# Optimization experiments

Measured on AMD Instinct MI355X. Metric: run time of the kernel, lower is better.

Reference implementation:

```python
import jax, jax.numpy as jnp
import numpy as np

V, E, U, L = 50000, 512, 20, 9   # vocab, embed dim, user feats, labels
R, S, T = 64, 32, 50             # reviews, sentences/review, tokens/sentence
D = E + U                        # product-encoder input dim


def setup_inputs() -> dict:
    key = jax.random.key(0)
    ks = jax.random.split(key, 16)
    sc = lambda k, shape: (jax.random.normal(k, shape, jnp.float32) * 0.02)
    return {
        "inputs": jax.random.randint(ks[0], (R, S, T), 0, V),
        "user_feats": jax.random.normal(ks[1], (R, U), jnp.float32),
        "embedding": sc(ks[2], (V, E)),
        "w_sent": sc(ks[3], (E, E)), "b_sent": jnp.zeros((E,), jnp.float32),
        "w_rev": sc(ks[4], (E, E)),  "b_rev": jnp.zeros((E,), jnp.float32),
        "w_prod": sc(ks[5], (D, D)), "b_prod": jnp.zeros((D,), jnp.float32),
        "w_rff": sc(ks[6], (D, 1)),  "b_rff": jnp.zeros((1,), jnp.float32),
        "w_pff": sc(ks[7], (D, L)),  "b_pff": jnp.zeros((L,), jnp.float32),
        "user_w": jnp.ones((U,), jnp.float32),
    }


def _masked_mean(x, mask):
    # x: [..., N, F], mask: [..., N] -> [..., F]
    denom = jnp.maximum(mask.sum(-1, keepdims=True), 1.0)
    return (x * mask[..., None]).sum(-2) / denom


def reference(inputs, user_feats, embedding, w_sent, b_sent, w_rev, b_rev,
              w_prod, b_prod, w_rff, b_rff, w_pff, b_pff, user_w):
    dt = embedding.dtype
    tok_mask = (inputs != 0).astype(dt)                      # [R,S,T]
    emb = embedding[inputs]                                  # [R,S,T,E]
    # sentence encoder (DAN): masked mean over tokens + Linear + SELU
    sent_h = jax.nn.selu(_masked_mean(emb, tok_mask) @ w_sent + b_sent)   # [R,S,E]
    # review encoder: masked mean over sentences (r_mask = p.sum(-1) != 0)
    sent_mask = (inputs.sum(-1) != 0).astype(dt)             # [R,S]
    rev_h = jax.nn.selu(_masked_mean(sent_h, sent_mask) @ w_rev + b_rev)  # [R,E]
    # append L2-normalized user feats scaled by learned weights
    norm = jnp.sqrt((user_feats * user_feats).sum(-1, keepdims=True))
    uf = user_feats / jnp.maximum(norm, 1e-12) * user_w      # [R,U]
    p_batch = jnp.concatenate([rev_h, uf], axis=-1)          # [R,D]
    # per-review star head
    r_stars = jax.nn.selu(p_batch @ w_rff + b_rff).squeeze(-1)            # [R]
    # product encoder: plain mean over reviews (no mask) + Linear + SELU
    h_n = jax.nn.selu(p_batch.mean(-2) @ w_prod + b_prod)    # [D]
    p_stars = jax.nn.selu(h_n @ w_pff + b_pff)               # [L]
    return p_stars, r_stars
```

## Files before the change

kernel.cpp:

```cpp
#include <hip/hip_runtime.h>
#include <hip/hip_bf16.h>

#define R_ 64
#define S_ 32
#define T_ 50
#define E_ 512
#define U_ 20
#define D_ 532
#define L_ 9
#define NSENT (R_ * S_)

#define PCHUNK 128
#define NCG 5
#define NKG 5

typedef __attribute__((ext_vector_type(8))) short bf16x8;
typedef __attribute__((ext_vector_type(4))) float f32x4;

__device__ __forceinline__ float selu_f(float x) {
    const float scale = 1.0507009873554805f;
    const float alpha = 1.6732632423543772f;
    return x > 0.0f ? scale * x : scale * alpha * expm1f(x);
}

__device__ __forceinline__ void store_out(float* p, float v) { *p = v; }
__device__ __forceinline__ void store_out(__hip_bfloat16* p, float v) { *p = __float2bfloat16(v); }

__global__ __launch_bounds__(256) void k_sent_mean(
        const int* __restrict__ inputs,
        const float* __restrict__ emb,
        __hip_bfloat16* __restrict__ sent_bf,
        float* __restrict__ smask)
{
    const int sid = blockIdx.x;
    const int tid = threadIdx.x;
    const int base = sid * T_;
    float2 acc = {0.f, 0.f};
    int cnt = 0;
    int idsum = 0;
    for (int t = 0; t < T_; ++t) {
        int tok = inputs[base + t];
        idsum += tok;
        if (tok != 0) {
            ++cnt;
            float2 v = ((const float2*)(emb + (size_t)tok * E_))[tid];
            acc.x += v.x; acc.y += v.y;
        }
    }
    const float denom = fmaxf((float)cnt, 1.0f);
    __hip_bfloat162 h2;
    h2.x = __float2bfloat16(acc.x / denom);
    h2.y = __float2bfloat16(acc.y / denom);
    ((__hip_bfloat162*)(sent_bf + (size_t)sid * E_))[tid] = h2;
    if (tid == 0) smask[sid] = (idsum != 0) ? 1.0f : 0.0f;
}

__global__ __launch_bounds__(256) void k_cvt_wT(
        const float* __restrict__ w_sent,
        const float* __restrict__ w_rev,
        __hip_bfloat16* __restrict__ wT)
{
    const float* w = blockIdx.z ? w_rev : w_sent;
    __hip_bfloat16* o = wT + (size_t)blockIdx.z * E_ * E_;
    __shared__ float tile[32][33];
    const int tx = threadIdx.x & 31, ty = threadIdx.x >> 5;
    const int k0 = blockIdx.y * 32, n0 = blockIdx.x * 32;
    #pragma unroll
    for (int i = 0; i < 4; ++i)
        tile[ty + 8 * i][tx] = w[(size_t)(k0 + ty + 8 * i) * E_ + n0 + tx];
    __syncthreads();
    #pragma unroll
    for (int i = 0; i < 4; ++i)
        o[(size_t)(n0 + ty + 8 * i) * E_ + k0 + tx] = __float2bfloat16(tile[tx][ty + 8 * i]);
}

template <typename OutT>
__global__ __launch_bounds__(256) void k_gemm_selu(
        const __hip_bfloat16* __restrict__ A,
        const __hip_bfloat16* __restrict__ Bt,
        const float* __restrict__ bias,
        OutT* __restrict__ C, int ldc)
{
    __shared__ short As[64][40];
    __shared__ short Bs[64][40];
    const int tid  = threadIdx.x;
    const int wid  = tid >> 6;
    const int lane = tid & 63;
    const int wm = wid >> 1, wn = wid & 1;
    const int bm = blockIdx.y * 64, bn = blockIdx.x * 64;

    const int srow = tid >> 2;
    const int soff = (tid & 3) * 8;

    const short* Ag  = (const short*)A;
    const short* Btg = (const short*)Bt;

    f32x4 acc[2][2];
    #pragma unroll
    for (int i = 0; i < 2; ++i)
        #pragma unroll
        for (int j = 0; j < 2; ++j) acc[i][j] = (f32x4){0.f, 0.f, 0.f, 0.f};

    const int fr = lane & 15;
    const int kg = (lane >> 4) * 8;

    for (int k0 = 0; k0 < E_; k0 += 32) {
        __syncthreads();
        *(bf16x8*)&As[srow][soff] = *(const bf16x8*)&Ag[(size_t)(bm + srow) * E_ + k0 + soff];
        *(bf16x8*)&Bs[srow][soff] = *(const bf16x8*)&Btg[(size_t)(bn + srow) * E_ + k0 + soff];
        __syncthreads();
        bf16x8 af0 = *(const bf16x8*)&As[wm * 32 + fr][kg];
        bf16x8 af1 = *(const bf16x8*)&As[wm * 32 + 16 + fr][kg];
        bf16x8 bf0 = *(const bf16x8*)&Bs[wn * 32 + fr][kg];
        bf16x8 bf1 = *(const bf16x8*)&Bs[wn * 32 + 16 + fr][kg];
        acc[0][0] = __builtin_amdgcn_mfma_f32_16x16x32_bf16(af0, bf0, acc[0][0], 0, 0, 0);
        acc[0][1] = __builtin_amdgcn_mfma_f32_16x16x32_bf16(af0, bf1, acc[0][1], 0, 0, 0);
        acc[1][0] = __builtin_amdgcn_mfma_f32_16x16x32_bf16(af1, bf0, acc[1][0], 0, 0, 0);
        acc[1][1] = __builtin_amdgcn_mfma_f32_16x16x32_bf16(af1, bf1, acc[1][1], 0, 0, 0);
    }

    const int rq = (lane >> 4) * 4;
    #pragma unroll
    for (int fm = 0; fm < 2; ++fm) {
        #pragma unroll
        for (int fn = 0; fn < 2; ++fn) {
            const int col = bn + wn * 32 + fn * 16 + fr;
            const float bv = bias[col];
            #pragma unroll
            for (int j = 0; j < 4; ++j) {
                const int row = bm + wm * 32 + fm * 16 + rq + j;
                store_out(&C[(size_t)row * ldc + col], selu_f(acc[fm][fn][j] + bv));
            }
        }
    }
}

__global__ __launch_bounds__(256) void k_rev_mean(
        const __hip_bfloat16* __restrict__ sent_h,
        const float* __restrict__ smask,
        __hip_bfloat16* __restrict__ mrev)
{
    const int r = blockIdx.x;
    const int tid = threadIdx.x;
    float2 acc = {0.f, 0.f};
    float msum = 0.f;
    for (int s = 0; s < S_; ++s) {
        const float m = smask[r * S_ + s];
        __hip_bfloat162 v = ((const __hip_bfloat162*)(sent_h + (size_t)(r * S_ + s) * E_))[tid];
        acc.x = fmaf(__bfloat162float(v.x), m, acc.x);
        acc.y = fmaf(__bfloat162float(v.y), m, acc.y);
        msum += m;
    }
    const float denom = fmaxf(msum, 1.0f);
    __hip_bfloat162 h2;
    h2.x = __float2bfloat16(acc.x / denom);
    h2.y = __float2bfloat16(acc.y / denom);
    ((__hip_bfloat162*)(mrev + (size_t)r * E_))[tid] = h2;
}

__global__ __launch_bounds__(64) void k_pbatch(
        const float* __restrict__ user_feats,
        const float* __restrict__ user_w,
        const float* __restrict__ w_rff,
        const float* __restrict__ b_rff,
        float* __restrict__ p_batch,
        float* __restrict__ out_r)
{
    __shared__ float uf[U_];
    const int r = blockIdx.x;
    const int tid = threadIdx.x;
    if (tid < U_) {
        float ss = 0.f;
        #pragma unroll
        for (int j = 0; j < U_; ++j) {
            const float u = user_feats[r * U_ + j];
            ss = fmaf(u, u, ss);
        }
        const float nrm = fmaxf(sqrtf(ss), 1e-12f);
        const float v = user_feats[r * U_ + tid] / nrm * user_w[tid];
        uf[tid] = v;
        p_batch[(size_t)r * D_ + E_ + tid] = v;
    }
    __syncthreads();
    float part = 0.f;
    #pragma unroll
    for (int i = 0; i < 8; ++i)
        part = fmaf(p_batch[(size_t)r * D_ + tid + 64 * i], w_rff[tid + 64 * i], part);
    if (tid < U_) part = fmaf(uf[tid], w_rff[E_ + tid], part);
    #pragma unroll
    for (int off = 32; off > 0; off >>= 1) part += __shfl_down(part, off, 64);
    if (tid == 0) out_r[r] = selu_f(part + b_rff[0]);
}

__global__ __launch_bounds__(256) void k_prod_partial(
        const float* __restrict__ p_batch,
        const float* __restrict__ w_prod,
        float* __restrict__ part)
{
    __shared__ float pbar[PCHUNK];
    __shared__ float red[2][PCHUNK];
    const int cg = blockIdx.x, kg = blockIdx.y;
    const int tid = threadIdx.x;
    const int cl = tid & (PCHUNK - 1);
    const int h  = tid >> 7;
    const int k0 = kg * PCHUNK;
    const int klen = min(PCHUNK, D_ - k0);

    if (cl < klen) {
        float s = 0.f;
        #pragma unroll 8
        for (int r = h * 32; r < h * 32 + 32; ++r)
            s += p_batch[(size_t)r * D_ + k0 + cl];
        red[h][cl] = s;
    }
    __syncthreads();
    if (h == 0 && cl < klen) pbar[cl] = (red[0][cl] + red[1][cl]) * (1.0f / 64.0f);
    __syncthreads();

    const int c = cg * PCHUNK + cl;
    float acc = 0.f;
    if (c < D_) {
        const int jb = h * 64;
        const int je = min(jb + 64, klen);
        for (int j = jb; j < je; ++j)
            acc = fmaf(pbar[j], w_prod[(size_t)(k0 + j) * D_ + c], acc);
    }
    red[h][cl] = acc;
    __syncthreads();
    if (h == 0 && c < D_) part[kg * D_ + c] = red[0][cl] + red[1][cl];
}

__global__ __launch_bounds__(256) void k_prod_final(
        const float* __restrict__ part,
        const float* __restrict__ b_prod,
        const float* __restrict__ w_pff,
        const float* __restrict__ b_pff,
        float* __restrict__ out_p)
{
    __shared__ float hn[D_];
    const int tid = threadIdx.x;
    for (int c = tid; c < D_; c += 256) {
        float s = b_prod[c];
        #pragma unroll
        for (int kg = 0; kg < NKG; ++kg) s += part[kg * D_ + c];
        hn[c] = selu_f(s);
    }
    __syncthreads();
    if (tid < L_) {
        float a = 0.f;
        for (int k = 0; k < D_; ++k) a = fmaf(hn[k], w_pff[k * L_ + tid], a);
        out_p[tid] = selu_f(a + b_pff[tid]);
    }
}

extern "C" void kernel_launch(void* const* d_in, const int* in_sizes, int n_in,
                              void* d_out, int out_size, void* d_ws, size_t ws_size,
                              hipStream_t stream) {
    const int*   inputs     = (const int*)  d_in[0];
    const float* user_feats = (const float*)d_in[1];
    const float* emb        = (const float*)d_in[2];
    const float* w_sent     = (const float*)d_in[3];
    const float* b_sent     = (const float*)d_in[4];
    const float* w_rev      = (const float*)d_in[5];
    const float* b_rev      = (const float*)d_in[6];
    const float* w_prod     = (const float*)d_in[7];
    const float* b_prod     = (const float*)d_in[8];
    const float* w_rff      = (const float*)d_in[9];
    const float* b_rff      = (const float*)d_in[10];
    const float* w_pff      = (const float*)d_in[11];
    const float* b_pff      = (const float*)d_in[12];
    const float* user_w     = (const float*)d_in[13];
    float* out = (float*)d_out;

    float* ws = (float*)d_ws;
    __hip_bfloat16* sent_bf  = (__hip_bfloat16*)(ws);
    __hip_bfloat16* sent_hbf = (__hip_bfloat16*)(ws + 524288);
    __hip_bfloat16* wT       = (__hip_bfloat16*)(ws + 1048576);
    __hip_bfloat16* mrev     = (__hip_bfloat16*)(ws + 1310720);
    float* smask   = ws + 1327104;
    float* p_batch = ws + 1329152;
    float* part    = ws + 1363200;

    k_sent_mean<<<NSENT, 256, 0, stream>>>(inputs, emb, sent_bf, smask);
    k_cvt_wT<<<dim3(16, 16, 2), 256, 0, stream>>>(w_sent, w_rev, wT);
    k_gemm_selu<__hip_bfloat16><<<dim3(E_ / 64, NSENT / 64), 256, 0, stream>>>(
        sent_bf, wT, b_sent, sent_hbf, E_);
    k_rev_mean<<<R_, 256, 0, stream>>>(sent_hbf, smask, mrev);
    k_gemm_selu<float><<<dim3(E_ / 64, R_ / 64), 256, 0, stream>>>(
        mrev, wT + (size_t)E_ * E_, b_rev, p_batch, D_);
    k_pbatch<<<R_, 64, 0, stream>>>(user_feats, user_w, w_rff, b_rff, p_batch, out + L_);
    k_prod_partial<<<dim3(NCG, NKG), 256, 0, stream>>>(p_batch, w_prod, part);
    k_prod_final<<<1, 256, 0, stream>>>(part, b_prod, w_pff, b_pff, out);
}
```

Before: 81.89 us.

## Fuse sentence mean with weight transpose and fold review GEMM into review kernel

```diff
diff --git a/kernel.cpp b/kernel.cpp
--- a/kernel.cpp
+++ b/kernel.cpp
@@ -23,63 +23,72 @@
     return x > 0.0f ? scale * x : scale * alpha * expm1f(x);
 }
 
-__device__ __forceinline__ void store_out(float* p, float v) { *p = v; }
-__device__ __forceinline__ void store_out(__hip_bfloat16* p, float v) { *p = __float2bfloat16(v); }
-
-__global__ __launch_bounds__(256) void k_sent_mean(
+__global__ __launch_bounds__(256) void k_fused_A(
         const int* __restrict__ inputs,
         const float* __restrict__ emb,
+        const float* __restrict__ w_sent,
         __hip_bfloat16* __restrict__ sent_bf,
+        __hip_bfloat16* __restrict__ wT,
         float* __restrict__ smask)
 {
+    __shared__ float red[2][E_];
+    __shared__ int scnt[2], ssum[2];
+    __shared__ float tile[32][33];
+    const int tid = threadIdx.x;
+
+    if (blockIdx.x >= NSENT) {
+        const int b = blockIdx.x - NSENT;
+        const int tx = tid & 31, ty = tid >> 5;
+        const int k0 = (b >> 4) * 32, n0 = (b & 15) * 32;
+        #pragma unroll
+        for (int i = 0; i < 4; ++i)
+            tile[ty + 8 * i][tx] = w_sent[(size_t)(k0 + ty + 8 * i) * E_ + n0 + tx];
+        __syncthreads();
+        #pragma unroll
+        for (int i = 0; i < 4; ++i)
+            wT[(size_t)(n0 + ty + 8 * i) * E_ + k0 + tx] = __float2bfloat16(tile[tx][ty + 8 * i]);
+        return;
+    }
+
     const int sid = blockIdx.x;
-    const int tid = threadIdx.x;
-    const int base = sid * T_;
-    float2 acc = {0.f, 0.f};
-    int cnt = 0;
-    int idsum = 0;
-    for (int t = 0; t < T_; ++t) {
-        int tok = inputs[base + t];
+    const int c4 = (tid & 127) * 4;
+    const int half = tid >> 7;
+    float4 acc = {0.f, 0.f, 0.f, 0.f};
+    int cnt = 0, idsum = 0;
+    #pragma unroll
+    for (int t = half; t < T_; t += 2) {
+        const int tok = inputs[sid * T_ + t];
+        const float m = (tok != 0) ? 1.0f : 0.0f;
+        cnt += (tok != 0);
         idsum += tok;
-        if (tok != 0) {
-            ++cnt;
-            float2 v = ((const float2*)(emb + (size_t)tok * E_))[tid];
-            acc.x += v.x; acc.y += v.y;
-        }
-    }
-    const float denom = fmaxf((float)cnt, 1.0f);
-    __hip_bfloat162 h2;
-    h2.x = __float2bfloat16(acc.x / denom);
-    h2.y = __float2bfloat16(acc.y / denom);
-    ((__hip_bfloat162*)(sent_bf + (size_t)sid * E_))[tid] = h2;
-    if (tid == 0) smask[sid] = (idsum != 0) ? 1.0f : 0.0f;
-}
-
-__global__ __launch_bounds__(256) void k_cvt_wT(
-        const float* __restrict__ w_sent,
-        const float* __restrict__ w_rev,
-        __hip_bfloat16* __restrict__ wT)
-{
-    const float* w = blockIdx.z ? w_rev : w_sent;
-    __hip_bfloat16* o = wT + (size_t)blockIdx.z * E_ * E_;
-    __shared__ float tile[32][33];
-    const int tx = threadIdx.x & 31, ty = threadIdx.x >> 5;
-    const int k0 = blockIdx.y * 32, n0 = blockIdx.x * 32;
-    #pragma unroll
-    for (int i = 0; i < 4; ++i)
-        tile[ty + 8 * i][tx] = w[(size_t)(k0 + ty + 8 * i) * E_ + n0 + tx];
-    __syncthreads();
-    #pragma unroll
-    for (int i = 0; i < 4; ++i)
-        o[(size_t)(n0 + ty + 8 * i) * E_ + k0 + tx] = __float2bfloat16(tile[tx][ty + 8 * i]);
-}
-
-template <typename OutT>
+        const float4 v = *(const float4*)(emb + (size_t)tok * E_ + c4);
+        acc.x = fmaf(v.x, m, acc.x);
+        acc.y = fmaf(v.y, m, acc.y);
+        acc.z = fmaf(v.z, m, acc.z);
+        acc.w = fmaf(v.w, m, acc.w);
+    }
+    *(float4*)&red[half][c4] = acc;
+    if ((tid & 127) == 0) { scnt[half] = cnt; ssum[half] = idsum; }
+    __syncthreads();
+    if (half == 0) {
+        const float4 a = *(const float4*)&red[0][c4];
+        const float4 b = *(const float4*)&red[1][c4];
+        const float inv = 1.0f / fmaxf((float)(scnt[0] + scnt[1]), 1.0f);
+        union { ushort4 u; __hip_bfloat16 h[4]; } o;
+        o.h[0] = __float2bfloat16((a.x + b.x) * inv);
+        o.h[1] = __float2bfloat16((a.y + b.y) * inv);
+        o.h[2] = __float2bfloat16((a.z + b.z) * inv);
+        o.h[3] = __float2bfloat16((a.w + b.w) * inv);
+        *((ushort4*)(sent_bf + (size_t)sid * E_) + (tid & 127)) = o.u;
+        if (tid == 0) smask[sid] = ((ssum[0] + ssum[1]) != 0) ? 1.0f : 0.0f;
+    }
+}
+
 __global__ __launch_bounds__(256) void k_gemm_selu(
         const __hip_bfloat16* __restrict__ A,
         const __hip_bfloat16* __restrict__ Bt,
         const float* __restrict__ bias,
-        OutT* __restrict__ C, int ldc)
+        __hip_bfloat16* __restrict__ C, int ldc)
 {
     __shared__ short As[64][40];
     __shared__ short Bs[64][40];
@@ -129,36 +138,17 @@
             #pragma unroll
             for (int j = 0; j < 4; ++j) {
                 const int row = bm + wm * 32 + fm * 16 + rq + j;
-                store_out(&C[(size_t)row * ldc + col], selu_f(acc[fm][fn][j] + bv));
+                C[(size_t)row * ldc + col] = __float2bfloat16(selu_f(acc[fm][fn][j] + bv));
             }
         }
     }
 }
 
-__global__ __launch_bounds__(256) void k_rev_mean(
+__global__ __launch_bounds__(256) void k_rev_fused(
         const __hip_bfloat16* __restrict__ sent_h,
         const float* __restrict__ smask,
-        __hip_bfloat16* __restrict__ mrev)
-{
-    const int r = blockIdx.x;
-    const int tid = threadIdx.x;
-    float2 acc = {0.f, 0.f};
-    float msum = 0.f;
-    for (int s = 0; s < S_; ++s) {
-        const float m = smask[r * S_ + s];
-        __hip_bfloat162 v = ((const __hip_bfloat162*)(sent_h + (size_t)(r * S_ + s) * E_))[tid];
-        acc.x = fmaf(__bfloat162float(v.x), m, acc.x);
-        acc.y = fmaf(__bfloat162float(v.y), m, acc.y);
-        msum += m;
-    }
-    const float denom = fmaxf(msum, 1.0f);
-    __hip_bfloat162 h2;
-    h2.x = __float2bfloat16(acc.x / denom);
-    h2.y = __float2bfloat16(acc.y / denom);
-    ((__hip_bfloat162*)(mrev + (size_t)r * E_))[tid] = h2;
-}
-
-__global__ __launch_bounds__(64) void k_pbatch(
+        const float* __restrict__ w_rev,
+        const float* __restrict__ b_rev,
         const float* __restrict__ user_feats,
         const float* __restrict__ user_w,
         const float* __restrict__ w_rff,
@@ -166,9 +156,35 @@
         float* __restrict__ p_batch,
         float* __restrict__ out_r)
 {
-    __shared__ float uf[U_];
+    __shared__ float mrow[E_];
+    __shared__ float prow[D_];
+    __shared__ float wsum[4];
     const int r = blockIdx.x;
     const int tid = threadIdx.x;
+
+    float2 acc = {0.f, 0.f};
+    float msum = 0.f;
+    for (int s = 0; s < S_; ++s) {
+        const float m = smask[r * S_ + s];
+        const __hip_bfloat162 v = ((const __hip_bfloat162*)(sent_h + (size_t)(r * S_ + s) * E_))[tid];
+        acc.x = fmaf(__bfloat162float(v.x), m, acc.x);
+        acc.y = fmaf(__bfloat162float(v.y), m, acc.y);
+        msum += m;
+    }
+    const float inv = 1.0f / fmaxf(msum, 1.0f);
+    mrow[2 * tid]     = acc.x * inv;
+    mrow[2 * tid + 1] = acc.y * inv;
+    __syncthreads();
+
+    float a0 = 0.f, a1 = 0.f;
+    for (int k = 0; k < E_; ++k) {
+        const float xv = mrow[k];
+        a0 = fmaf(xv, w_rev[(size_t)k * E_ + tid], a0);
+        a1 = fmaf(xv, w_rev[(size_t)k * E_ + tid + 256], a1);
+    }
+    prow[tid]       = selu_f(a0 + b_rev[tid]);
+    prow[tid + 256] = selu_f(a1 + b_rev[tid + 256]);
+
     if (tid < U_) {
         float ss = 0.f;
         #pragma unroll
@@ -177,19 +193,24 @@
             ss = fmaf(u, u, ss);
         }
         const float nrm = fmaxf(sqrtf(ss), 1e-12f);
-        const float v = user_feats[r * U_ + tid] / nrm * user_w[tid];
-        uf[tid] = v;
-        p_batch[(size_t)r * D_ + E_ + tid] = v;
-    }
-    __syncthreads();
+        prow[E_ + tid] = user_feats[r * U_ + tid] / nrm * user_w[tid];
+    }
+    __syncthreads();
+
+    p_batch[(size_t)r * D_ + tid]       = prow[tid];
+    p_batch[(size_t)r * D_ + tid + 256] = prow[tid + 256];
+    if (tid < D_ - 512) p_batch[(size_t)r * D_ + 512 + tid] = prow[512 + tid];
+
     float part = 0.f;
-    #pragma unroll
-    for (int i = 0; i < 8; ++i)
-        part = fmaf(p_batch[(size_t)r * D_ + tid + 64 * i], w_rff[tid + 64 * i], part);
-    if (tid < U_) part = fmaf(uf[tid], w_rff[E_ + tid], part);
+    for (int k = tid; k < D_; k += 256) part = fmaf(prow[k], w_rff[k], part);
     #pragma unroll
     for (int off = 32; off > 0; off >>= 1) part += __shfl_down(part, off, 64);
-    if (tid == 0) out_r[r] = selu_f(part + b_rff[0]);
+    if ((tid & 63) == 0) wsum[tid >> 6] = part;
+    __syncthreads();
+    if (tid == 0) {
+        const float tot = wsum[0] + wsum[1] + wsum[2] + wsum[3];
+        out_r[r] = selu_f(tot + b_rff[0]);
+    }
 }
 
 __global__ __launch_bounds__(256) void k_prod_partial(
@@ -276,19 +297,15 @@
     __hip_bfloat16* sent_bf  = (__hip_bfloat16*)(ws);
     __hip_bfloat16* sent_hbf = (__hip_bfloat16*)(ws + 524288);
     __hip_bfloat16* wT       = (__hip_bfloat16*)(ws + 1048576);
-    __hip_bfloat16* mrev     = (__hip_bfloat16*)(ws + 1310720);
-    float* smask   = ws + 1327104;
-    float* p_batch = ws + 1329152;
-    float* part    = ws + 1363200;
-
-    k_sent_mean<<<NSENT, 256, 0, stream>>>(inputs, emb, sent_bf, smask);
-    k_cvt_wT<<<dim3(16, 16, 2), 256, 0, stream>>>(w_sent, w_rev, wT);
-    k_gemm_selu<__hip_bfloat16><<<dim3(E_ / 64, NSENT / 64), 256, 0, stream>>>(
+    float* smask   = ws + 1179648;
+    float* p_batch = ws + 1181696;
+    float* part    = ws + 1215744;
+
+    k_fused_A<<<NSENT + 256, 256, 0, stream>>>(inputs, emb, w_sent, sent_bf, wT, smask);
+    k_gemm_selu<<<dim3(E_ / 64, NSENT / 64), 256, 0, stream>>>(
         sent_bf, wT, b_sent, sent_hbf, E_);
-    k_rev_mean<<<R_, 256, 0, stream>>>(sent_hbf, smask, mrev);
-    k_gemm_selu<float><<<dim3(E_ / 64, R_ / 64), 256, 0, stream>>>(
-        mrev, wT + (size_t)E_ * E_, b_rev, p_batch, D_);
-    k_pbatch<<<R_, 64, 0, stream>>>(user_feats, user_w, w_rff, b_rff, p_batch, out + L_);
+    k_rev_fused<<<R_, 256, 0, stream>>>(sent_hbf, smask, w_rev, b_rev, user_feats, user_w,
+                                        w_rff, b_rff, p_batch, out + L_);
     k_prod_partial<<<dim3(NCG, NKG), 256, 0, stream>>>(p_batch, w_prod, part);
     k_prod_final<<<1, 256, 0, stream>>>(part, b_prod, w_pff, b_pff, out);
 }
```

Result: slower. 94.83 us (+15.8%).
